# Kernel optimization log

Measured on AMD Instinct MI355X. Metric: run time of the kernel, lower is better.

Reference implementation:

```python
import jax, jax.numpy as jnp
import numpy as np

T, B, C = 2048, 4, 512
H, K, P = 16, 31, 15  # num_heads, kernel_size, padding_l
R = C // H


def setup_inputs() -> dict:
    key = jax.random.key(0)
    ks = jax.random.split(key, 6)
    x = jax.random.normal(ks[0], (T, B, C), dtype=jnp.float32)
    s = 0.02
    W1 = jax.random.normal(ks[1], (C, C), dtype=jnp.float32) * s   # linear1 weight
    b1 = jnp.zeros((C,), dtype=jnp.float32)
    Wl = jax.random.normal(ks[2], (H * K, C), dtype=jnp.float32) * s  # weight_linear (no bias)
    W2 = jax.random.normal(ks[3], (C, C), dtype=jnp.float32) * s   # linear2 weight
    b2 = jnp.zeros((C,), dtype=jnp.float32)
    return {"x": x, "W1": W1, "b1": b1, "Wl": Wl, "W2": W2, "b2": b2}


def _dynamic_conv(h, Wl):
    # h: (T, B, C). Generate per-position per-head filters, softmax over K,
    # then banded weighted sum over a local window of K timesteps.
    w = jnp.einsum('tbc,kc->tbk', h, Wl).reshape(T, B, H, K)
    w = jax.nn.softmax(w, axis=-1)                      # weight_softmax=True
    # pad left P, right K-1-P ("same" window: position t sees h[t-P : t-P+K])
    hp = jnp.pad(h, ((P, K - 1 - P), (0, 0), (0, 0)))   # (T+K-1, B, C)
    idx = jnp.arange(T)[:, None] + jnp.arange(K)[None, :]  # (T, K)
    hw = hp[idx].reshape(T, K, B, H, R)                 # unfolded windows
    return jnp.einsum('tkbhr,tbhk->tbhr', hw, w).reshape(T, B, C)


def reference(x, W1, b1, Wl, W2, b2):
    h = jnp.einsum('tbc,dc->tbd', x, W1) + b1           # linear1 (glu=False -> no act)
    out = _dynamic_conv(h, Wl)                          # conv_bias=False
    out = jnp.einsum('tbc,dc->tbd', out, W2) + b2       # linear2
    return out
```

## Files before the change

### kernel.cpp

```cpp
#include <hip/hip_runtime.h>
#include <hip/hip_bf16.h>

#define TT 2048
#define BB 4
#define CC 512
#define HH 16
#define KK 31
#define PP 15
#define MM (TT*BB)
#define NPAD 512

typedef __bf16 bf16x8 __attribute__((ext_vector_type(8)));
typedef float f32x4 __attribute__((ext_vector_type(4)));
typedef unsigned short ushort8 __attribute__((ext_vector_type(8)));
typedef unsigned short ushort4v __attribute__((ext_vector_type(4)));

__device__ __forceinline__ float bf2f(unsigned short u) {
    return __uint_as_float(((unsigned int)u) << 16);
}
__device__ __forceinline__ unsigned short f2bf(float f) {
    unsigned int x = __float_as_uint(f);
    x += 0x7fffu + ((x >> 16) & 1u);
    return (unsigned short)(x >> 16);
}

__global__ __launch_bounds__(256) void cast_x(const float* __restrict__ src,
                                              unsigned short* __restrict__ dst) {
    const int i = (blockIdx.x * 256 + threadIdx.x) * 4;
    const float4 v = *(const float4*)&src[i];
    ushort4v o = { f2bf(v.x), f2bf(v.y), f2bf(v.z), f2bf(v.w) };
    *(ushort4v*)&dst[i] = o;
}

__global__ __launch_bounds__(256) void cast_weights(const float* __restrict__ W1,
                                                    const float* __restrict__ Wl,
                                                    const float* __restrict__ W2,
                                                    unsigned short* __restrict__ W1b,
                                                    unsigned short* __restrict__ Wlb,
                                                    unsigned short* __restrict__ W2b) {
    const int b = blockIdx.x;
    const int i = (b & 255) * 1024 + threadIdx.x * 4;
    const float* src;
    unsigned short* dst;
    int n_src = 262144;
    if (b < 256)      { src = W1; dst = W1b; }
    else if (b < 512) { src = Wl; dst = Wlb; n_src = HH * KK * CC; }
    else              { src = W2; dst = W2b; }
    ushort4v o = {0, 0, 0, 0};
    if (i < n_src) {
        const float4 v = *(const float4*)&src[i];
        o[0] = f2bf(v.x); o[1] = f2bf(v.y); o[2] = f2bf(v.z); o[3] = f2bf(v.w);
    }
    *(ushort4v*)&dst[i] = o;
}

#define GBM 128
#define GBN 64
#define GBK 64

template<bool OUT_BF16>
__global__ __launch_bounds__(256, 2) void gemm_nt_mfma(const unsigned short* __restrict__ A,
                                                       const unsigned short* __restrict__ B,
                                                       const float* __restrict__ bias,
                                                       void* __restrict__ Cout,
                                                       int N, int Kc, int nn) {
    __shared__ short As[2][GBM * GBK];
    __shared__ short Bs[2][GBN * GBK];

    const int tid = threadIdx.x;
    const int l   = tid & 63;
    const int wv  = tid >> 6;
    const int wr  = wv >> 1;
    const int wc  = wv & 1;

    const int s  = (blockIdx.x & 7) * (gridDim.x >> 3) + (blockIdx.x >> 3);
    const int bm = (s / nn) * GBM;
    const int bn = (s % nn) * GBN;

    const unsigned short* gA[4];
    const unsigned short* gB[2];
    #pragma unroll
    for (int j = 0; j < 4; ++j) {
        const int idx16 = j * 256 + tid;
        const int r  = idx16 >> 3;
        const int sl = (idx16 & 7) ^ (r & 7);
        gA[j] = A + (size_t)(bm + r) * Kc + sl * 8;
    }
    #pragma unroll
    for (int j = 0; j < 2; ++j) {
        const int idx16 = j * 256 + tid;
        const int r  = idx16 >> 3;
        const int sl = (idx16 & 7) ^ (r & 7);
        gB[j] = B + (size_t)(bn + r) * Kc + sl * 8;
    }

    f32x4 acc[4][2] = {};

    const int lr = l & 15;
    const int ls = l >> 4;
    int offA[4][2], offB[2][2];
    #pragma unroll
    for (int mi = 0; mi < 4; ++mi) {
        const int r = wr * 64 + mi * 16 + lr;
        #pragma unroll
        for (int ks = 0; ks < 2; ++ks)
            offA[mi][ks] = r * 64 + (((ks * 4 + ls) ^ (r & 7)) * 8);
    }
    #pragma unroll
    for (int ni = 0; ni < 2; ++ni) {
        const int r = wc * 32 + ni * 16 + lr;
        #pragma unroll
        for (int ks = 0; ks < 2; ++ks)
            offB[ni][ks] = r * 64 + (((ks * 4 + ls) ^ (r & 7)) * 8);
    }

    const int NT = Kc / GBK;

    #pragma unroll
    for (int j = 0; j < 4; ++j)
        __builtin_amdgcn_global_load_lds((const __attribute__((address_space(1))) void*)(gA[j]),
                                         (__attribute__((address_space(3))) void*)(&As[0][0] + j * 2048 + wv * 512), 16, 0, 0);
    #pragma unroll
    for (int j = 0; j < 2; ++j)
        __builtin_amdgcn_global_load_lds((const __attribute__((address_space(1))) void*)(gB[j]),
                                         (__attribute__((address_space(3))) void*)(&Bs[0][0] + j * 2048 + wv * 512), 16, 0, 0);
    __syncthreads();

    int cur = 0;
    for (int kt = 0; kt < NT; ++kt) {
        if (kt + 1 < NT) {
            const int k0 = (kt + 1) * GBK;
            #pragma unroll
            for (int j = 0; j < 4; ++j)
                __builtin_amdgcn_global_load_lds((const __attribute__((address_space(1))) void*)(gA[j] + k0),
                                                 (__attribute__((address_space(3))) void*)(&As[cur ^ 1][0] + j * 2048 + wv * 512), 16, 0, 0);
            #pragma unroll
            for (int j = 0; j < 2; ++j)
                __builtin_amdgcn_global_load_lds((const __attribute__((address_space(1))) void*)(gB[j] + k0),
                                                 (__attribute__((address_space(3))) void*)(&Bs[cur ^ 1][0] + j * 2048 + wv * 512), 16, 0, 0);
        }

        bf16x8 af[4][2], bfv[2][2];
        #pragma unroll
        for (int mi = 0; mi < 4; ++mi)
            #pragma unroll
            for (int ks = 0; ks < 2; ++ks)
                af[mi][ks] = *(const bf16x8*)&As[cur][offA[mi][ks]];
        #pragma unroll
        for (int ni = 0; ni < 2; ++ni)
            #pragma unroll
            for (int ks = 0; ks < 2; ++ks)
                bfv[ni][ks] = *(const bf16x8*)&Bs[cur][offB[ni][ks]];

        #pragma unroll
        for (int mi = 0; mi < 4; ++mi)
            #pragma unroll
            for (int ni = 0; ni < 2; ++ni)
                #pragma unroll
                for (int ks = 0; ks < 2; ++ks)
                    acc[mi][ni] = __builtin_amdgcn_mfma_f32_16x16x32_bf16(af[mi][ks], bfv[ni][ks], acc[mi][ni], 0, 0, 0);

        __syncthreads();
        cur ^= 1;
    }

    #pragma unroll
    for (int mi = 0; mi < 4; ++mi) {
        const int row0 = bm + wr * 64 + mi * 16 + ls * 4;
        #pragma unroll
        for (int ni = 0; ni < 2; ++ni) {
            const int col = bn + wc * 32 + ni * 16 + lr;
            const float bv = bias ? bias[col] : 0.0f;
            #pragma unroll
            for (int j = 0; j < 4; ++j) {
                const float v = acc[mi][ni][j] + bv;
                if (OUT_BF16)
                    ((unsigned short*)Cout)[(size_t)(row0 + j) * N + col] = f2bf(v);
                else
                    ((float*)Cout)[(size_t)(row0 + j) * N + col] = v;
            }
        }
    }
}

__global__ __launch_bounds__(256) void dynconv_fused(const unsigned short* __restrict__ hb,
                                                     const unsigned short* __restrict__ logits,
                                                     unsigned short* __restrict__ cvb) {
    __shared__ float w_s[64][33];

    const int bid = blockIdx.x;
    const int t   = (bid & 7) * 256 + (bid >> 3);
    const int tid = threadIdx.x;

    {
        const int r = tid >> 2;
        const int q = tid & 3;
        const int b = r >> 4, hd = r & 15;
        const unsigned short* lp = logits + (size_t)(t * BB + b) * NPAD + hd * KK;
        float e[8];
        const int k0 = q * 8;
        const int kn = (q == 3) ? 7 : 8;
        float mx = -1e30f;
        #pragma unroll
        for (int j = 0; j < 8; ++j) {
            e[j] = (j < kn) ? bf2f(lp[k0 + j]) : -1e30f;
            mx = fmaxf(mx, e[j]);
        }
        mx = fmaxf(mx, __shfl_xor(mx, 1, 4));
        mx = fmaxf(mx, __shfl_xor(mx, 2, 4));
        float sm = 0.f;
        #pragma unroll
        for (int j = 0; j < 8; ++j) {
            e[j] = (j < kn) ? __expf(e[j] - mx) : 0.f;
            sm += e[j];
        }
        sm += __shfl_xor(sm, 1, 4);
        sm += __shfl_xor(sm, 2, 4);
        const float inv = 1.f / sm;
        #pragma unroll
        for (int j = 0; j < 8; ++j)
            if (j < kn) w_s[r][k0 + j] = e[j] * inv;
    }
    __syncthreads();

    const int c0 = (tid & 63) * 8;
    const int b  = tid >> 6;
    const int wrow = b * 16 + (c0 >> 5);
    float acc[8] = {};
    #pragma unroll
    for (int k = 0; k < KK; ++k) {
        const int tt = t - PP + k;
        if ((unsigned)tt >= TT) continue;
        const ushort8 hv = *(const ushort8*)&hb[(size_t)((tt * BB + b) * CC) + c0];
        const float wk = w_s[wrow][k];
        #pragma unroll
        for (int j = 0; j < 8; ++j) acc[j] = fmaf(bf2f(hv[j]), wk, acc[j]);
    }
    ushort8 o;
    #pragma unroll
    for (int j = 0; j < 8; ++j) o[j] = f2bf(acc[j]);
    *(ushort8*)&cvb[(size_t)((t * BB + b) * CC) + c0] = o;
}

extern "C" void kernel_launch(void* const* d_in, const int* in_sizes, int n_in,
                              void* d_out, int out_size, void* d_ws, size_t ws_size,
                              hipStream_t stream) {
    const float* x  = (const float*)d_in[0];
    const float* W1 = (const float*)d_in[1];
    const float* b1 = (const float*)d_in[2];
    const float* Wl = (const float*)d_in[3];
    const float* W2 = (const float*)d_in[4];
    const float* b2 = (const float*)d_in[5];
    float* out = (float*)d_out;

    unsigned short* xb  = (unsigned short*)d_ws;
    unsigned short* hb  = xb  + (size_t)MM * CC;
    unsigned short* cvb = hb  + (size_t)MM * CC;
    unsigned short* W1b = cvb + (size_t)MM * CC;
    unsigned short* Wlb = W1b + (size_t)CC * CC;
    unsigned short* W2b = Wlb + (size_t)NPAD * CC;
    unsigned short* lgb = W2b + (size_t)CC * CC;

    const int nxc = MM * CC;

    cast_x<<<nxc / 1024, 256, 0, stream>>>(x, xb);
    cast_weights<<<768, 256, 0, stream>>>(W1, Wl, W2, W1b, Wlb, W2b);

    const int nblk = (MM / GBM) * (CC / GBN);

    gemm_nt_mfma<true><<<nblk, 256, 0, stream>>>(xb, W1b, b1, hb, CC, CC, CC / GBN);
    gemm_nt_mfma<true><<<nblk, 256, 0, stream>>>(hb, Wlb, nullptr, lgb, NPAD, CC, NPAD / GBN);
    dynconv_fused<<<TT, 256, 0, stream>>>(hb, lgb, cvb);
    gemm_nt_mfma<false><<<nblk, 256, 0, stream>>>(cvb, W2b, b2, out, CC, CC, CC / GBN);
}
```

Before: 60.61 us.

## Triple-buffer GEMM LDS staging with vmcnt waits and one barrier per step

Changes the bf16 MFMA GEMM from double buffering to triple buffering in LDS, issuing loads two k-tiles ahead. Each iteration now waits on vmcnt and a single barrier instead of a full __syncthreads after compute. The K dimension is fixed at compile time so the loop fully unrolls. LDS use rises to 72KB per block, which may hold occupancy at the 2 blocks per CU the launch bounds ask for. The wait relies on exact vmcnt accounting of the six global_load_lds issues per stage.

```diff
diff --git a/kernel.cpp b/kernel.cpp
--- a/kernel.cpp
+++ b/kernel.cpp
@@ -57,15 +57,34 @@
 #define GBM 128
 #define GBN 64
 #define GBK 64
+#define KC  512
+#define NT  8
+
+#define STAGE(kt, buf)                                                                         \
+    do {                                                                                       \
+        const int k0_ = (kt) * GBK;                                                            \
+        _Pragma("unroll")                                                                      \
+        for (int j = 0; j < 4; ++j)                                                            \
+            __builtin_amdgcn_global_load_lds(                                                  \
+                (const __attribute__((address_space(1))) void*)(gA[j] + k0_),                  \
+                (__attribute__((address_space(3))) void*)(&As[buf][0] + j * 2048 + wv * 512),  \
+                16, 0, 0);                                                                     \
+        _Pragma("unroll")                                                                      \
+        for (int j = 0; j < 2; ++j)                                                            \
+            __builtin_amdgcn_global_load_lds(                                                  \
+                (const __attribute__((address_space(1))) void*)(gB[j] + k0_),                  \
+                (__attribute__((address_space(3))) void*)(&Bs[buf][0] + j * 2048 + wv * 512),  \
+                16, 0, 0);                                                                     \
+    } while (0)
 
 template<bool OUT_BF16>
 __global__ __launch_bounds__(256, 2) void gemm_nt_mfma(const unsigned short* __restrict__ A,
                                                        const unsigned short* __restrict__ B,
                                                        const float* __restrict__ bias,
                                                        void* __restrict__ Cout,
-                                                       int N, int Kc, int nn) {
-    __shared__ short As[2][GBM * GBK];
-    __shared__ short Bs[2][GBN * GBK];
+                                                       int N, int nn) {
+    __shared__ short As[3][GBM * GBK];
+    __shared__ short Bs[3][GBN * GBK];
 
     const int tid = threadIdx.x;
     const int l   = tid & 63;
@@ -84,14 +103,14 @@
         const int idx16 = j * 256 + tid;
         const int r  = idx16 >> 3;
         const int sl = (idx16 & 7) ^ (r & 7);
-        gA[j] = A + (size_t)(bm + r) * Kc + sl * 8;
+        gA[j] = A + (size_t)(bm + r) * KC + sl * 8;
     }
     #pragma unroll
     for (int j = 0; j < 2; ++j) {
         const int idx16 = j * 256 + tid;
         const int r  = idx16 >> 3;
         const int sl = (idx16 & 7) ^ (r & 7);
-        gB[j] = B + (size_t)(bn + r) * Kc + sl * 8;
+        gB[j] = B + (size_t)(bn + r) * KC + sl * 8;
     }
 
     f32x4 acc[4][2] = {};
@@ -114,43 +133,28 @@
             offB[ni][ks] = r * 64 + (((ks * 4 + ls) ^ (r & 7)) * 8);
     }
 
-    const int NT = Kc / GBK;
-
-    #pragma unroll
-    for (int j = 0; j < 4; ++j)
-        __builtin_amdgcn_global_load_lds((const __attribute__((address_space(1))) void*)(gA[j]),
-                                         (__attribute__((address_space(3))) void*)(&As[0][0] + j * 2048 + wv * 512), 16, 0, 0);
-    #pragma unroll
-    for (int j = 0; j < 2; ++j)
-        __builtin_amdgcn_global_load_lds((const __attribute__((address_space(1))) void*)(gB[j]),
-                                         (__attribute__((address_space(3))) void*)(&Bs[0][0] + j * 2048 + wv * 512), 16, 0, 0);
-    __syncthreads();
-
-    int cur = 0;
+    STAGE(0, 0);
+    STAGE(1, 1);
+
+    #pragma unroll
     for (int kt = 0; kt < NT; ++kt) {
-        if (kt + 1 < NT) {
-            const int k0 = (kt + 1) * GBK;
-            #pragma unroll
-            for (int j = 0; j < 4; ++j)
-                __builtin_amdgcn_global_load_lds((const __attribute__((address_space(1))) void*)(gA[j] + k0),
-                                                 (__attribute__((address_space(3))) void*)(&As[cur ^ 1][0] + j * 2048 + wv * 512), 16, 0, 0);
-            #pragma unroll
-            for (int j = 0; j < 2; ++j)
-                __builtin_amdgcn_global_load_lds((const __attribute__((address_space(1))) void*)(gB[j] + k0),
-                                                 (__attribute__((address_space(3))) void*)(&Bs[cur ^ 1][0] + j * 2048 + wv * 512), 16, 0, 0);
-        }
-
+        if (kt < NT - 1) asm volatile("s_waitcnt vmcnt(6)" ::: "memory");
+        else             asm volatile("s_waitcnt vmcnt(0)" ::: "memory");
+        __builtin_amdgcn_s_barrier();
+        if (kt + 2 < NT) STAGE(kt + 2, (kt + 2) % 3);
+
+        const int cb = kt % 3;
         bf16x8 af[4][2], bfv[2][2];
         #pragma unroll
         for (int mi = 0; mi < 4; ++mi)
             #pragma unroll
             for (int ks = 0; ks < 2; ++ks)
-                af[mi][ks] = *(const bf16x8*)&As[cur][offA[mi][ks]];
+                af[mi][ks] = *(const bf16x8*)&As[cb][offA[mi][ks]];
         #pragma unroll
         for (int ni = 0; ni < 2; ++ni)
             #pragma unroll
             for (int ks = 0; ks < 2; ++ks)
-                bfv[ni][ks] = *(const bf16x8*)&Bs[cur][offB[ni][ks]];
+                bfv[ni][ks] = *(const bf16x8*)&Bs[cb][offB[ni][ks]];
 
         #pragma unroll
         for (int mi = 0; mi < 4; ++mi)
@@ -159,9 +163,6 @@
                 #pragma unroll
                 for (int ks = 0; ks < 2; ++ks)
                     acc[mi][ni] = __builtin_amdgcn_mfma_f32_16x16x32_bf16(af[mi][ks], bfv[ni][ks], acc[mi][ni], 0, 0, 0);
-
-        __syncthreads();
-        cur ^= 1;
     }
 
     #pragma unroll
@@ -268,8 +269,8 @@
 
     const int nblk = (MM / GBM) * (CC / GBN);
 
-    gemm_nt_mfma<true><<<nblk, 256, 0, stream>>>(xb, W1b, b1, hb, CC, CC, CC / GBN);
-    gemm_nt_mfma<true><<<nblk, 256, 0, stream>>>(hb, Wlb, nullptr, lgb, NPAD, CC, NPAD / GBN);
+    gemm_nt_mfma<true><<<nblk, 256, 0, stream>>>(xb, W1b, b1, hb, CC, CC / GBN);
+    gemm_nt_mfma<true><<<nblk, 256, 0, stream>>>(hb, Wlb, nullptr, lgb, NPAD, NPAD / GBN);
     dynconv_fused<<<TT, 256, 0, stream>>>(hb, lgb, cvb);
-    gemm_nt_mfma<false><<<nblk, 256, 0, stream>>>(cvb, W2b, b2, out, CC, CC, CC / GBN);
-}
+    gemm_nt_mfma<false><<<nblk, 256, 0, stream>>>(cvb, W2b, b2, out, CC, CC / GBN);
+}
```

Result: faster. 55.66 us (-8.2%).
